# Performance work log

Hardware: AMD Instinct MI355X
Metric: run time of the kernel (lower is better)

The kernel has to match this reference:

```python
import jax, jax.numpy as jnp
import numpy as np

NUM_HEADS = 12


def _get_rel_pos(q_size, k_size, rel_pos):
    # q_size == k_size here, so the torch interpolate branch is never taken;
    # table already has 2*max(q,k)-1 rows. Gather by relative coordinate.
    coords = jnp.arange(q_size)[:, None] - jnp.arange(k_size)[None, :] + (k_size - 1)
    return rel_pos[coords]  # (q_size, k_size, head_dim)


def setup_inputs() -> dict:
    key = jax.random.key(0)
    ks = jax.random.split(key, 8)
    B, D, H, W, dim = 32, 8, 8, 8, 768
    hd = dim // NUM_HEADS
    s = 0.02
    return {
        "x": jax.random.normal(ks[0], (B, D, H, W, dim), jnp.float32),
        "w_qkv": jax.random.normal(ks[1], (dim, 3 * dim), jnp.float32) * s,
        "b_qkv": jnp.zeros((3 * dim,), jnp.float32),
        "w_proj": jax.random.normal(ks[2], (dim, dim), jnp.float32) * s,
        "b_proj": jnp.zeros((dim,), jnp.float32),
        "rel_pos_d": jax.random.normal(ks[3], (2 * D - 1, hd), jnp.float32) * s,
        "rel_pos_h": jax.random.normal(ks[4], (2 * H - 1, hd), jnp.float32) * s,
        "rel_pos_w": jax.random.normal(ks[5], (2 * W - 1, hd), jnp.float32) * s,
    }


def reference(x, w_qkv, b_qkv, w_proj, b_proj, rel_pos_d, rel_pos_h, rel_pos_w):
    B, D, H, W, dim = x.shape
    nH = NUM_HEADS
    hd = dim // nH
    N = D * H * W
    scale = hd ** -0.5

    # qkv projection: (B, N, 3, nH, hd) -> (3, B*nH, N, hd)
    qkv = (x.reshape(B, N, dim) @ w_qkv + b_qkv).reshape(B, N, 3, nH, hd)
    qkv = jnp.transpose(qkv, (2, 0, 3, 1, 4)).reshape(3, B * nH, N, hd)
    q, k, v = qkv[0], qkv[1], qkv[2]

    attn = jnp.einsum('bqc,bkc->bqk', q * scale, k)  # (B*nH, N, N)

    # decomposed relative positional bias (MViTv2-style)
    Rd = _get_rel_pos(D, D, rel_pos_d)  # (D, D, hd)
    Rh = _get_rel_pos(H, H, rel_pos_h)  # (H, H, hd)
    Rw = _get_rel_pos(W, W, rel_pos_w)  # (W, W, hd)
    r_q = q.reshape(B * nH, D, H, W, hd)
    rel_d = jnp.einsum('bdhwc,dkc->bdhwk', r_q, Rd)
    rel_h = jnp.einsum('bdhwc,hkc->bdhwk', r_q, Rh)
    rel_w = jnp.einsum('bdhwc,wkc->bdhwk', r_q, Rw)

    attn = attn.reshape(B * nH, D, H, W, D, H, W)
    attn = (attn
            + rel_d[:, :, :, :, :, None, None]
            + rel_h[:, :, :, :, None, :, None]
            + rel_w[:, :, :, :, None, None, :])
    attn = jax.nn.softmax(attn.reshape(B * nH, N, N), axis=-1)

    out = (attn @ v).reshape(B, nH, D, H, W, hd)
    out = jnp.transpose(out, (0, 2, 3, 4, 1, 5)).reshape(B, D, H, W, dim)
    return out @ w_proj + b_proj
```

## Files before the change

### kernel.cpp

```cpp
#include <hip/hip_runtime.h>
#include <hip/hip_bf16.h>
#include <cstdint>

typedef __bf16 bf16x8 __attribute__((ext_vector_type(8)));
typedef __bf16 bf16x4 __attribute__((ext_vector_type(4)));
typedef float  f32x4  __attribute__((ext_vector_type(4)));
typedef float  f32x16 __attribute__((ext_vector_type(16)));
typedef unsigned u32x4 __attribute__((ext_vector_type(4)));

__device__ __forceinline__ f32x4 mfma16(bf16x8 a, bf16x8 b, f32x4 c) {
  return __builtin_amdgcn_mfma_f32_16x16x32_bf16(a, b, c, 0, 0, 0);
}
__device__ __forceinline__ f32x16 mfma32(bf16x8 a, bf16x8 b, f32x16 c) {
  return __builtin_amdgcn_mfma_f32_32x32x16_bf16(a, b, c, 0, 0, 0);
}

__device__ __forceinline__ void gload_lds16(const __bf16* g, __bf16* l) {
  __builtin_amdgcn_global_load_lds(
      (const __attribute__((address_space(1))) void*)g,
      (__attribute__((address_space(3))) void*)l, 16, 0, 0);
}

__device__ __forceinline__ unsigned cvtpk(float lo, float hi) {
  unsigned r;
  asm("v_cvt_pk_bf16_f32 %0, %1, %2" : "=v"(r) : "v"(lo), "v"(hi));
  return r;
}
__device__ __forceinline__ void plswap(unsigned& a, unsigned& b) {
  asm("v_permlane32_swap_b32 %0, %1" : "+v"(a), "+v"(b));
}

__global__ __launch_bounds__(256) void cvt_bf16_kernel(const float* __restrict__ in,
                                                       __bf16* __restrict__ out, int n4) {
  int i = blockIdx.x * 256 + threadIdx.x;
  if (i < n4) {
    float4 v = ((const float4*)in)[i];
    bf16x4 o;
    o[0] = (__bf16)v.x; o[1] = (__bf16)v.y; o[2] = (__bf16)v.z; o[3] = (__bf16)v.w;
    ((bf16x4*)out)[i] = o;
  }
}

__global__ __launch_bounds__(256) void transpose_cvt_kernel(const float* __restrict__ src,
                                                            __bf16* __restrict__ dst,
                                                            int R, int C) {
  __shared__ float tile[32][33];
  int r0 = blockIdx.y * 32, c0 = blockIdx.x * 32;
  int tx = threadIdx.x & 31, ty = threadIdx.x >> 5;
#pragma unroll
  for (int i = 0; i < 4; ++i)
    tile[ty + i * 8][tx] = src[(size_t)(r0 + ty + i * 8) * C + c0 + tx];
  __syncthreads();
#pragma unroll
  for (int i = 0; i < 4; ++i) {
    int rr = ty + i * 8;
    dst[(size_t)(c0 + rr) * R + r0 + tx] = (__bf16)tile[tx][rr];
  }
}

template <int EPI>
__global__ __launch_bounds__(512) void gemm_bt2_kernel(
    const __bf16* __restrict__ A, const __bf16* __restrict__ Bt,
    int M, int N, int K, int nbx,
    const float* __restrict__ bias,
    float* __restrict__ outF,
    __bf16* __restrict__ qo, __bf16* __restrict__ ko, __bf16* __restrict__ vTo) {
  __shared__ __attribute__((aligned(16))) __bf16 lA[2][256 * 32];
  __shared__ __attribute__((aligned(16))) __bf16 lB[2][128 * 32];
  const int t = threadIdx.x;
  const int l = t & 63, w = t >> 6;
  const int wm = (w >> 1) * 64, wn = (w & 1) * 64;
  const int cpx = gridDim.x >> 3;
  const int wg = (blockIdx.x & 7) * cpx + (blockIdx.x >> 3);
  const int m0 = (wg / nbx) * 256, n0 = (wg % nbx) * 128;
  const int nk = K >> 5;

  auto stage = [&](int buf, int kt) {
    const __bf16* As = A + (size_t)m0 * K + kt * 32;
    const __bf16* Bs = Bt + (size_t)n0 * K + kt * 32;
#pragma unroll
    for (int rnd = 0; rnd < 2; ++rnd) {
      int li = rnd * 512 + t;
      int row = li >> 2, c8 = (li & 3) * 8;
      gload_lds16(As + (size_t)row * K + c8, &lA[buf][li * 8]);
    }
    {
      int row = t >> 2, c8 = (t & 3) * 8;
      gload_lds16(Bs + (size_t)row * K + c8, &lB[buf][t * 8]);
    }
  };

  f32x4 acc[4][4] = {};
  stage(0, 0);
  stage(1, 1);

  for (int kt = 0; kt < nk; ++kt) {
    asm volatile("s_waitcnt vmcnt(3)" ::: "memory");
    __builtin_amdgcn_s_barrier();
    __builtin_amdgcn_sched_barrier(0);
    const __bf16* la = &lA[kt & 1][0];
    const __bf16* lb = &lB[kt & 1][0];
    bf16x8 af[4], bfv[4];
#pragma unroll
    for (int mt = 0; mt < 4; ++mt)
      af[mt] = *(const bf16x8*)(la + (wm + mt * 16 + (l & 15)) * 32 + (l >> 4) * 8);
#pragma unroll
    for (int nt = 0; nt < 4; ++nt)
      bfv[nt] = *(const bf16x8*)(lb + (wn + nt * 16 + (l & 15)) * 32 + (l >> 4) * 8);
#pragma unroll
    for (int mt = 0; mt < 4; ++mt)
#pragma unroll
      for (int nt = 0; nt < 4; ++nt)
        acc[mt][nt] = mfma16(af[mt], bfv[nt], acc[mt][nt]);
    __builtin_amdgcn_sched_barrier(0);
    __builtin_amdgcn_s_barrier();
    __builtin_amdgcn_sched_barrier(0);
    int nxt = kt + 2 < nk ? kt + 2 : nk - 1;
    stage(kt & 1, nxt);
  }

#pragma unroll
  for (int mt = 0; mt < 4; ++mt) {
#pragma unroll
    for (int nt = 0; nt < 4; ++nt) {
#pragma unroll
      for (int r = 0; r < 4; ++r) {
        int row = m0 + wm + mt * 16 + (l >> 4) * 4 + r;
        int col = n0 + wn + nt * 16 + (l & 15);
        float val = acc[mt][nt][r] + bias[col];
        if constexpr (EPI == 0) {
          int s = col / 768, rem = col - s * 768;
          int h = rem >> 6, c = rem & 63;
          int b = row >> 9, n = row & 511;
          size_t bh = (size_t)(b * 12 + h);
          __bf16 bv = (__bf16)val;
          if (s == 0)      qo[(bh * 512 + n) * 64 + c] = bv;
          else if (s == 1) ko[(bh * 512 + n) * 64 + c] = bv;
          else             vTo[(bh * 64 + c) * 512 + n] = bv;
        } else {
          outF[(size_t)row * N + col] = val;
        }
      }
    }
  }
}

__device__ __forceinline__ const bf16x8* kfrag(const __bf16* base, int row, int ch) {
  return (const bf16x8*)(base + row * 64 + ((ch ^ (row & 7)) * 8));
}
__device__ __forceinline__ const bf16x8* vfrag(const __bf16* base, int row, int ch) {
  return (const bf16x8*)(base + row * 32 + ((ch ^ ((row >> 1) & 3)) * 8));
}

__global__ __launch_bounds__(256, 4) void attn_kernel(
    const __bf16* __restrict__ qg_, const __bf16* __restrict__ kg,
    const __bf16* __restrict__ vT,
    const float* __restrict__ rpd, const float* __restrict__ rph,
    const float* __restrict__ rpw,
    __bf16* __restrict__ attn_out) {
  const int bid = (blockIdx.x & 7) * 192 + (blockIdx.x >> 3);
  const int bh = bid >> 2;
  const int qb = bid & 3;
  const int t = threadIdx.x, w = t >> 6, l = t & 63;
  const int lq = l & 31, lh5 = l >> 5;

  __shared__ float bias_lds[128][25];
  __shared__ float rs_lds[4][32];
  __shared__ __attribute__((aligned(16))) __bf16 k_lds[2][32 * 64];
  __shared__ __attribute__((aligned(16))) __bf16 v_lds[2][64 * 32];

  const __bf16* kb = kg + (size_t)bh * 512 * 64;
  const __bf16* vb = vT + (size_t)bh * 64 * 512;

  auto stage = [&](int sbuf, int j0) {
    {
      int row = t >> 3, pc = t & 7;
      int lc = pc ^ (row & 7);
      gload_lds16(kb + (size_t)(j0 + row) * 64 + lc * 8, &k_lds[sbuf][t * 8]);
    }
    {
      int row = t >> 2, pc = t & 3;
      int lc = pc ^ ((row >> 1) & 3);
      gload_lds16(vb + (size_t)row * 512 + j0 + lc * 8, &v_lds[sbuf][t * 8]);
    }
  };

  stage(0, 0);

  const __bf16* qbase = qg_ + ((size_t)bh * 512 + qb * 128 + w * 32) * 64;
  bf16x8 qf[4];
#pragma unroll
  for (int s = 0; s < 4; ++s)
    qf[s] = *(const bf16x8*)(qbase + lq * 64 + s * 16 + lh5 * 8);

  {
    const int row = w * 32 + lq;
    const int n = qb * 128 + row;
    const int dd = n >> 6, hh = (n >> 3) & 7, ww = n & 7;
#pragma unroll
    for (int jt = 0; jt < 2; ++jt) {
      const float* src;
      if (jt == 0) src = (lq < 15) ? rpd + (size_t)lq * 64
                                   : (lq >= 16 && lq < 31) ? rph + (size_t)(lq - 16) * 64
                                                           : nullptr;
      else         src = (lq < 15) ? rpw + (size_t)lq * 64 : nullptr;
      f32x16 cb = {};
#pragma unroll
      for (int s = 0; s < 4; ++s) {
        bf16x8 afr;
        if (src) {
          float4 a = *(const float4*)(src + s * 16 + lh5 * 8);
          float4 b = *(const float4*)(src + s * 16 + lh5 * 8 + 4);
          u32x4 u = {cvtpk(a.x, a.y), cvtpk(a.z, a.w), cvtpk(b.x, b.y), cvtpk(b.z, b.w)};
          afr = __builtin_bit_cast(bf16x8, u);
        } else {
          afr = bf16x8{};
        }
        cb = mfma32(afr, qf[s], cb);
      }
#pragma unroll
      for (int r = 0; r < 16; ++r) {
        int j = (r & 3) + 8 * (r >> 2) + 4 * lh5;
        if (jt == 0) {
          if (j < 16) {
            int idx = dd + 7 - j;
            if (idx >= 0 && idx < 8) bias_lds[row][idx] = cb[r];
          } else {
            int idx = hh + 7 - (j - 16);
            if (idx >= 0 && idx < 8) bias_lds[row][8 + idx] = cb[r];
          }
        } else {
          if (j < 16) {
            int idx = ww + 7 - j;
            if (idx >= 0 && idx < 8) bias_lds[row][16 + idx] = cb[r];
          }
        }
      }
    }
  }

  __syncthreads();

  const float LOG2E = 1.44269504f;
  const float* brow = &bias_lds[w * 32 + lq][0];
  float bh2e[4], bh2o[4], bw2[4];
#pragma unroll
  for (int rr = 0; rr < 4; ++rr) {
    bh2e[rr] = brow[8 + rr] * LOG2E;
    bh2o[rr] = brow[12 + rr] * LOG2E;
    bw2[rr] = brow[16 + rr + 4 * lh5] * LOG2E;
  }

  f32x16 accO0 = {}, accO1 = {};
  float rs4[4] = {0.f, 0.f, 0.f, 0.f};
  const float scale2 = 0.125f * LOG2E;

  for (int kk = 0; kk < 8; ++kk) {
#pragma unroll
    for (int par = 0; par < 2; ++par) {
      const int kb_i = kk * 2 + par;
      if (kb_i < 15) stage(par ^ 1, (kb_i + 1) * 32);
      const __bf16* kl = k_lds[par];
      const __bf16* vl = v_lds[par];

      f32x16 accS = {};
#pragma unroll
      for (int s = 0; s < 4; ++s)
        accS = mfma32(*kfrag(kl, lq, lh5 + 2 * s), qf[s], accS);

      float bd2 = brow[kb_i >> 1] * LOG2E;
      float pr[16];
#pragma unroll
      for (int rr = 0; rr < 4; ++rr) {
        float bsum = bd2 + (par ? bh2o[rr] : bh2e[rr]);
#pragma unroll
        for (int c = 0; c < 4; ++c) {
          int r = rr * 4 + c;
          float p = __builtin_amdgcn_exp2f(accS[r] * scale2 + bsum + bw2[c]);
          rs4[rr] += p;
          pr[r] = p;
        }
      }

      unsigned a0 = cvtpk(pr[0], pr[1]),   b0 = cvtpk(pr[4], pr[5]);
      unsigned a1 = cvtpk(pr[2], pr[3]),   b1 = cvtpk(pr[6], pr[7]);
      unsigned a2 = cvtpk(pr[8], pr[9]),   b2 = cvtpk(pr[12], pr[13]);
      unsigned a3 = cvtpk(pr[10], pr[11]), b3 = cvtpk(pr[14], pr[15]);
      plswap(a0, b0); plswap(a1, b1); plswap(a2, b2); plswap(a3, b3);
      u32x4 u0 = {a0, a1, b0, b1};
      u32x4 u1 = {a2, a3, b2, b3};
      bf16x8 pf0 = __builtin_bit_cast(bf16x8, u0);
      bf16x8 pf1 = __builtin_bit_cast(bf16x8, u1);

      accO0 = mfma32(pf0, *vfrag(vl, lq, lh5), accO0);
      accO0 = mfma32(pf1, *vfrag(vl, lq, lh5 + 2), accO0);
      accO1 = mfma32(pf0, *vfrag(vl, 32 + lq, lh5), accO1);
      accO1 = mfma32(pf1, *vfrag(vl, 32 + lq, lh5 + 2), accO1);

      __syncthreads();
    }
  }

  {
    float rsum = (rs4[0] + rs4[1]) + (rs4[2] + rs4[3]);
    float s = rsum + __shfl_xor(rsum, 32);
    if (l < 32) rs_lds[w][l] = 1.f / s;
  }

  const int b_ = bh / 12, h_ = bh - b_ * 12;
  __bf16* obase = attn_out + ((size_t)b_ * 512 + qb * 128 + w * 32) * 768 + h_ * 64;
#pragma unroll
  for (int rr = 0; rr < 4; ++rr) {
#pragma unroll
    for (int c = 0; c < 4; ++c) {
      int r = rr * 4 + c;
      int qrow = c + 8 * rr + 4 * lh5;
      float inv = rs_lds[w][qrow];
      obase[(size_t)qrow * 768 + lq]      = (__bf16)(accO0[r] * inv);
      obase[(size_t)qrow * 768 + 32 + lq] = (__bf16)(accO1[r] * inv);
    }
  }
}

extern "C" void kernel_launch(void* const* d_in, const int* in_sizes, int n_in,
                              void* d_out, int out_size, void* d_ws, size_t ws_size,
                              hipStream_t stream) {
  const float* x      = (const float*)d_in[0];
  const float* w_qkv  = (const float*)d_in[1];
  const float* b_qkv  = (const float*)d_in[2];
  const float* w_proj = (const float*)d_in[3];
  const float* b_proj = (const float*)d_in[4];
  const float* rpd    = (const float*)d_in[5];
  const float* rph    = (const float*)d_in[6];
  const float* rpw    = (const float*)d_in[7];
  float* out = (float*)d_out;

  char* base = (char*)d_ws;
  __bf16* xb     = (__bf16*)(base);
  __bf16* wqkvT  = (__bf16*)(base + 25165824);
  __bf16* wprojT = (__bf16*)(base + 25165824 + 3538944);
  __bf16* qb     = (__bf16*)(base + 25165824 + 3538944 + 1179648);
  __bf16* kb     = qb + (size_t)384 * 512 * 64;
  __bf16* vT     = kb + (size_t)384 * 512 * 64;

  cvt_bf16_kernel<<<12288, 256, 0, stream>>>(x, xb, 12582912 / 4);
  transpose_cvt_kernel<<<dim3(2304 / 32, 768 / 32), 256, 0, stream>>>(w_qkv, wqkvT, 768, 2304);
  transpose_cvt_kernel<<<dim3(768 / 32, 768 / 32), 256, 0, stream>>>(w_proj, wprojT, 768, 768);

  gemm_bt2_kernel<0><<<1152, 512, 0, stream>>>(
      xb, wqkvT, 16384, 2304, 768, 18, b_qkv, nullptr, qb, kb, vT);

  attn_kernel<<<1536, 256, 0, stream>>>(qb, kb, vT, rpd, rph, rpw, xb);

  gemm_bt2_kernel<1><<<384, 512, 0, stream>>>(
      xb, wprojT, 16384, 768, 768, 6, b_proj, out, nullptr, nullptr, nullptr);
}
```

Measured before the change: 205.2 us.

## Triple-buffer GEMM with BK=64, XOR-swizzled LDS, and split-phase prefetch

Reworks the bf16 GEMM mainloop to use three LDS buffers with a K-tile of 64 instead of two buffers of 32. LDS chunks are XOR-swizzled by row to avoid bank conflicts on the wider rows. Loads for tile j+2 are issued in two halves interleaved with the two MFMA sub-steps, and the MFMA bursts are wrapped in s_setprio. This drops one barrier per iteration and deepens prefetch, but LDS use rises to 144KB per block, which may reduce occupancy to one block per CU.

```diff
diff --git a/kernel.cpp b/kernel.cpp
--- a/kernel.cpp
+++ b/kernel.cpp
@@ -59,64 +59,74 @@
 }
 
 template <int EPI>
-__global__ __launch_bounds__(512) void gemm_bt2_kernel(
+__global__ __launch_bounds__(512) void gemm_bt3_kernel(
     const __bf16* __restrict__ A, const __bf16* __restrict__ Bt,
     int M, int N, int K, int nbx,
     const float* __restrict__ bias,
     float* __restrict__ outF,
     __bf16* __restrict__ qo, __bf16* __restrict__ ko, __bf16* __restrict__ vTo) {
-  __shared__ __attribute__((aligned(16))) __bf16 lA[2][256 * 32];
-  __shared__ __attribute__((aligned(16))) __bf16 lB[2][128 * 32];
+  __shared__ __attribute__((aligned(16))) __bf16 lA[3][256 * 64];
+  __shared__ __attribute__((aligned(16))) __bf16 lB[3][128 * 64];
   const int t = threadIdx.x;
   const int l = t & 63, w = t >> 6;
   const int wm = (w >> 1) * 64, wn = (w & 1) * 64;
   const int cpx = gridDim.x >> 3;
   const int wg = (blockIdx.x & 7) * cpx + (blockIdx.x >> 3);
   const int m0 = (wg / nbx) * 256, n0 = (wg % nbx) * 128;
-  const int nk = K >> 5;
-
-  auto stage = [&](int buf, int kt) {
-    const __bf16* As = A + (size_t)m0 * K + kt * 32;
-    const __bf16* Bs = Bt + (size_t)n0 * K + kt * 32;
-#pragma unroll
-    for (int rnd = 0; rnd < 2; ++rnd) {
-      int li = rnd * 512 + t;
-      int row = li >> 2, c8 = (li & 3) * 8;
-      gload_lds16(As + (size_t)row * K + c8, &lA[buf][li * 8]);
+  const int nk = K >> 6;
+
+  auto stage = [&](int buf, int kt, int part) {
+    const __bf16* As = A + (size_t)m0 * K + kt * 64;
+    const __bf16* Bs = Bt + (size_t)n0 * K + kt * 64;
+#pragma unroll
+    for (int r2 = 0; r2 < 2; ++r2) {
+      int li = (part * 2 + r2) * 512 + t;
+      int row = li >> 3, pc = li & 7, lc = pc ^ (row & 7);
+      gload_lds16(As + (size_t)row * K + lc * 8, &lA[buf][li * 8]);
     }
     {
-      int row = t >> 2, c8 = (t & 3) * 8;
-      gload_lds16(Bs + (size_t)row * K + c8, &lB[buf][t * 8]);
+      int li = part * 512 + t;
+      int row = li >> 3, pc = li & 7, lc = pc ^ (row & 7);
+      gload_lds16(Bs + (size_t)row * K + lc * 8, &lB[buf][li * 8]);
     }
   };
 
   f32x4 acc[4][4] = {};
-  stage(0, 0);
-  stage(1, 1);
-
-  for (int kt = 0; kt < nk; ++kt) {
-    asm volatile("s_waitcnt vmcnt(3)" ::: "memory");
+  stage(0, 0, 0); stage(0, 0, 1);
+  stage(1, 1, 0); stage(1, 1, 1);
+
+  for (int j = 0; j < nk; ++j) {
+    asm volatile("s_waitcnt vmcnt(6)" ::: "memory");
     __builtin_amdgcn_s_barrier();
     __builtin_amdgcn_sched_barrier(0);
-    const __bf16* la = &lA[kt & 1][0];
-    const __bf16* lb = &lB[kt & 1][0];
-    bf16x8 af[4], bfv[4];
-#pragma unroll
-    for (int mt = 0; mt < 4; ++mt)
-      af[mt] = *(const bf16x8*)(la + (wm + mt * 16 + (l & 15)) * 32 + (l >> 4) * 8);
-#pragma unroll
-    for (int nt = 0; nt < 4; ++nt)
-      bfv[nt] = *(const bf16x8*)(lb + (wn + nt * 16 + (l & 15)) * 32 + (l >> 4) * 8);
-#pragma unroll
-    for (int mt = 0; mt < 4; ++mt)
-#pragma unroll
-      for (int nt = 0; nt < 4; ++nt)
-        acc[mt][nt] = mfma16(af[mt], bfv[nt], acc[mt][nt]);
-    __builtin_amdgcn_sched_barrier(0);
-    __builtin_amdgcn_s_barrier();
-    __builtin_amdgcn_sched_barrier(0);
-    int nxt = kt + 2 < nk ? kt + 2 : nk - 1;
-    stage(kt & 1, nxt);
+    const __bf16* la = &lA[j % 3][0];
+    const __bf16* lb = &lB[j % 3][0];
+    const int st = (j + 2 < nk) ? j + 2 : j;
+    const int sb = (j + 2) % 3;
+#pragma unroll
+    for (int p = 0; p < 2; ++p) {
+      bf16x8 af[4], bfv[4];
+#pragma unroll
+      for (int mt = 0; mt < 4; ++mt) {
+        int row = wm + mt * 16 + (l & 15);
+        int ch = (p * 4 + (l >> 4)) ^ (row & 7);
+        af[mt] = *(const bf16x8*)(la + row * 64 + ch * 8);
+      }
+#pragma unroll
+      for (int nt = 0; nt < 4; ++nt) {
+        int row = wn + nt * 16 + (l & 15);
+        int ch = (p * 4 + (l >> 4)) ^ (row & 7);
+        bfv[nt] = *(const bf16x8*)(lb + row * 64 + ch * 8);
+      }
+      stage(sb, st, p);
+      __builtin_amdgcn_s_setprio(1);
+#pragma unroll
+      for (int mt = 0; mt < 4; ++mt)
+#pragma unroll
+        for (int nt = 0; nt < 4; ++nt)
+          acc[mt][nt] = mfma16(af[mt], bfv[nt], acc[mt][nt]);
+      __builtin_amdgcn_s_setprio(0);
+    }
   }
 
 #pragma unroll
@@ -347,11 +357,11 @@
   transpose_cvt_kernel<<<dim3(2304 / 32, 768 / 32), 256, 0, stream>>>(w_qkv, wqkvT, 768, 2304);
   transpose_cvt_kernel<<<dim3(768 / 32, 768 / 32), 256, 0, stream>>>(w_proj, wprojT, 768, 768);
 
-  gemm_bt2_kernel<0><<<1152, 512, 0, stream>>>(
+  gemm_bt3_kernel<0><<<1152, 512, 0, stream>>>(
       xb, wqkvT, 16384, 2304, 768, 18, b_qkv, nullptr, qb, kb, vT);
 
   attn_kernel<<<1536, 256, 0, stream>>>(qb, kb, vT, rpd, rph, rpw, xb);
 
-  gemm_bt2_kernel<1><<<384, 512, 0, stream>>>(
+  gemm_bt3_kernel<1><<<384, 512, 0, stream>>>(
       xb, wprojT, 16384, 768, 768, 6, b_proj, out, nullptr, nullptr, nullptr);
 }
```

Result: faster. 189.2 us (-7.8%).
